# Optimization experiments

Measured on AMD Instinct MI355X. Metric: run time of the kernel, lower is better.

The kernel has to match this reference:

```python
import jax, jax.numpy as jnp
import numpy as np

N, E, IN_DIM, HID = 50000, 800000, 128, 256
H2 = HID // 2
LN_EPS = 1e-5


def setup_inputs() -> dict:
    key = jax.random.key(0)
    ks = jax.random.split(key, 20)
    s = lambda k, shape, fan: jax.random.normal(k, shape, jnp.float32) * (1.0 / np.sqrt(fan))
    return {
        "x": jax.random.normal(ks[0], (N, IN_DIM), jnp.float32),
        "edge_index": jax.random.randint(ks[1], (2, E), 0, N, jnp.int64),
        # GATConv(in_dim, H2, heads=1, concat=False)
        "W_gat": s(ks[2], (IN_DIM, H2), IN_DIM),
        "att_src": s(ks[3], (H2,), H2),
        "att_dst": s(ks[4], (H2,), H2),
        "b_gat": jnp.zeros((H2,), jnp.float32),
        # SAGEConv(in_dim, H2): lin_l (with bias) on aggregated, lin_r (no bias) on root
        "W1l": s(ks[5], (IN_DIM, H2), IN_DIM),
        "b1l": jnp.zeros((H2,), jnp.float32),
        "W1r": s(ks[6], (IN_DIM, H2), IN_DIM),
        "ln1_g": jnp.ones((HID,), jnp.float32),
        "ln1_b": jnp.zeros((HID,), jnp.float32),
        # SAGEConv(hidden, hidden)
        "W2l": s(ks[7], (HID, HID), HID),
        "b2l": jnp.zeros((HID,), jnp.float32),
        "W2r": s(ks[8], (HID, HID), HID),
        "ln2_g": jnp.ones((HID,), jnp.float32),
        "ln2_b": jnp.zeros((HID,), jnp.float32),
        "Wc": s(ks[9], (HID, 1), HID),
        "bc": jnp.zeros((1,), jnp.float32),
    }


def _layernorm(h, g, b):
    mu = jnp.mean(h, axis=-1, keepdims=True)
    var = jnp.mean(jnp.square(h - mu), axis=-1, keepdims=True)
    return (h - mu) * jax.lax.rsqrt(var + LN_EPS) * g + b


def _sage(x, src, dst, Wl, bl, Wr, n):
    # mean aggregation of source features at destination, then lin_l(agg) + lin_r(x)
    s = jax.ops.segment_sum(x[src], dst, num_segments=n)
    deg = jax.ops.segment_sum(jnp.ones((src.shape[0],), x.dtype), dst, num_segments=n)
    agg = s / jnp.maximum(deg, 1.0)[:, None]
    return agg @ Wl + bl + x @ Wr


def _gat(x, src, dst, W, a_s, a_d, b, n):
    # heads=1, concat=False, add_self_loops=True, eval (no dropout)
    loop = jnp.arange(n)
    gs = jnp.concatenate([src, loop])
    gd = jnp.concatenate([dst, loop])
    h = x @ W                                  # [N, H2]
    e = jax.nn.leaky_relu(jnp.take(h @ a_s, gs) + jnp.take(h @ a_d, gd), 0.2)
    emax = jax.ops.segment_max(e, gd, num_segments=n)
    ex = jnp.exp(e - emax[gd])
    denom = jax.ops.segment_sum(ex, gd, num_segments=n)
    alpha = ex / denom[gd]                     # scatter-softmax over in-edges
    out = jax.ops.segment_sum(alpha[:, None] * h[gs], gd, num_segments=n)
    return out + b


def reference(x, edge_index, W_gat, att_src, att_dst, b_gat,
              W1l, b1l, W1r, ln1_g, ln1_b,
              W2l, b2l, W2r, ln2_g, ln2_b, Wc, bc):
    n = x.shape[0]
    src, dst = edge_index[0], edge_index[1]
    x1 = _gat(x, src, dst, W_gat, att_src, att_dst, b_gat, n)
    x2 = _sage(x, src, dst, W1l, b1l, W1r, n)
    h = jnp.concatenate([x1, x2], axis=-1)
    h = jax.nn.relu(_layernorm(h, ln1_g, ln1_b))
    h = _sage(h, src, dst, W2l, b2l, W2r, n)
    h = jax.nn.relu(_layernorm(h, ln2_g, ln2_b))
    return (h @ Wc + bc).squeeze(-1)
```

## Files before the change

### kernel.cpp

```cpp
#include <hip/hip_runtime.h>

#define LN_EPS 1e-5f
#define CA 2048
#define CAPB 6144

typedef __attribute__((ext_vector_type(8))) short short8;
typedef __attribute__((ext_vector_type(4))) float float4a;
typedef __attribute__((ext_vector_type(2))) float float2a;

__device__ __forceinline__ float lrelu(float v) { return v > 0.f ? v : 0.2f * v; }

__device__ __forceinline__ unsigned short f2bf(float f) {
    union { float f; unsigned int u; } x; x.f = f;
    unsigned int u = x.u;
    unsigned int r = (u + 0x7fffu + ((u >> 16) & 1u)) >> 16;
    return (unsigned short)r;
}
__device__ __forceinline__ float bflo(unsigned int v) {
    union { unsigned int u; float f; } x; x.u = v << 16; return x.f;
}
__device__ __forceinline__ float bfhi(unsigned int v) {
    union { unsigned int u; float f; } x; x.u = v & 0xffff0000u; return x.f;
}
__device__ __forceinline__ float2a bf2(unsigned int w) {
    union { unsigned int u; float f; } lo, hi;
    lo.u = w << 16; hi.u = w & 0xffff0000u;
    float2a r; r[0] = lo.f; r[1] = hi.f; return r;
}

__device__ __forceinline__ void load_lds16(const void* g, void* l) {
    __builtin_amdgcn_global_load_lds(
        (const __attribute__((address_space(1))) void*)g,
        (__attribute__((address_space(3))) void*)l, 16, 0, 0);
}

__device__ __forceinline__ uint4 ld16(const char* __restrict__ b, unsigned off) {
    return *(const uint4*)(b + off);
}

__device__ __forceinline__ void accb(float2a aw2[4], float2a ap2[4], float w, uint4 v) {
    float2a wm2; wm2[0] = w; wm2[1] = w;
    float2a f0 = bf2(v.x), f1 = bf2(v.y), f2v = bf2(v.z), f3 = bf2(v.w);
    aw2[0] += wm2 * f0; aw2[1] += wm2 * f1;
    aw2[2] += wm2 * f2v; aw2[3] += wm2 * f3;
    ap2[0] += f0; ap2[1] += f1;
    ap2[2] += f2v; ap2[3] += f3;
}

__device__ __forceinline__ void accbm(float2a aw2[4], float2a ap2[4], float wm, float sm, uint4 v) {
    float2a wm2; wm2[0] = wm; wm2[1] = wm;
    float2a sm2; sm2[0] = sm; sm2[1] = sm;
    float2a f0 = bf2(v.x), f1 = bf2(v.y), f2v = bf2(v.z), f3 = bf2(v.w);
    aw2[0] += wm2 * f0; aw2[1] += wm2 * f1;
    aw2[2] += wm2 * f2v; aw2[3] += wm2 * f3;
    ap2[0] += sm2 * f0; ap2[1] += sm2 * f1;
    ap2[2] += sm2 * f2v; ap2[3] += sm2 * f3;
}

__global__ void prep(const float* __restrict__ W_gat, const float* __restrict__ W1l,
                     const float* __restrict__ W1r, const float* __restrict__ W2l,
                     const float* __restrict__ W2r,
                     const float* __restrict__ att_s, const float* __restrict__ att_d,
                     unsigned short* __restrict__ W12T, unsigned short* __restrict__ W2cT,
                     float* __restrict__ vs, float* __restrict__ vd)
{
    int idx = blockIdx.x * 256 + threadIdx.x;
    if (idx < 98304) {
        int c = idx / 384, k = idx - c * 384;
        float v = 0.f;
        if (c < 128) { if (k < 128) v = W_gat[k * 128 + c]; }
        else {
            int cc = c - 128;
            if (k >= 256)       v = W1r[(k - 256) * 128 + cc];
            else if (k >= 128)  v = W1l[(k - 128) * 128 + cc];
        }
        W12T[idx] = f2bf(v);
    } else if (idx < 229376) {
        int t = idx - 98304;
        int c = t >> 9, k = t & 511;
        float v = (k < 256) ? W2l[k * 256 + c] : W2r[(k - 256) * 256 + c];
        W2cT[t] = f2bf(v);
    } else if (idx < 229376 + 128) {
        int k = idx - 229376;
        float s = 0.f, d = 0.f;
        for (int c = 0; c < 128; ++c) {
            float w = W_gat[k * 128 + c];
            s += w * att_s[c]; d += w * att_d[c];
        }
        vs[k] = s; vd[k] = d;
    }
}

__global__ __launch_bounds__(256) void conv_x_asad(
    const float* __restrict__ x, const float* __restrict__ vs, const float* __restrict__ vd,
    unsigned short* __restrict__ combo3, float* __restrict__ as_, float* __restrict__ ad_, int N)
{
    const int wave = threadIdx.x >> 6, lane = threadIdx.x & 63;
    const int i = blockIdx.x * 4 + wave;
    if (i >= N) return;
    float2 xv = *(const float2*)(x + (size_t)i * 128 + 2 * lane);
    float2 vsv = *(const float2*)(vs + 2 * lane);
    float2 vdv = *(const float2*)(vd + 2 * lane);
    float s = xv.x * vsv.x + xv.y * vsv.y;
    float d = xv.x * vdv.x + xv.y * vdv.y;
    #pragma unroll
    for (int off = 32; off > 0; off >>= 1) {
        s += __shfl_xor(s, off);
        d += __shfl_xor(d, off);
    }
    if (lane == 0) { as_[i] = s; ad_[i] = d; }
    unsigned pk = (unsigned)f2bf(xv.x) | ((unsigned)f2bf(xv.y) << 16);
    *(unsigned*)(combo3 + (size_t)i * 384 + 256 + 2 * lane) = pk;
}

__global__ __launch_bounds__(256) void radix_hist(
    const int* __restrict__ dst, int E, int* __restrict__ blockhist, int B)
{
    const int blk = blockIdx.x, t = threadIdx.x;
    __shared__ int hist[256];
    hist[t] = 0; __syncthreads();
    const int chunk = blk * CA, cend = min(chunk + CA, E);
    for (int j = chunk + t; j < cend; j += 256)
        atomicAdd(&hist[((unsigned)dst[j]) >> 8], 1);
    __syncthreads();
    blockhist[t * B + blk] = hist[t];
}

__global__ __launch_bounds__(256) void scan_rows(
    int* __restrict__ blockhist, int B, int* __restrict__ bintot)
{
    const int bin = blockIdx.x, t = threadIdx.x;
    __shared__ int tmp[256];
    __shared__ int carry;
    if (t == 0) carry = 0;
    __syncthreads();
    const int base = bin * B;
    for (int off0 = 0; off0 < B; off0 += 256) {
        int i = off0 + t;
        int v = (i < B) ? blockhist[base + i] : 0;
        tmp[t] = v; __syncthreads();
        for (int off = 1; off < 256; off <<= 1) {
            int a = (t >= off) ? tmp[t - off] : 0;
            __syncthreads();
            tmp[t] += a;
            __syncthreads();
        }
        int incl = tmp[t] + carry;
        if (i < B) blockhist[base + i] = incl - v;
        __syncthreads();
        if (t == 255) carry = incl;
        __syncthreads();
    }
    if (t == 0) bintot[bin] = carry;
}

__global__ __launch_bounds__(256) void scan_bins(
    const int* __restrict__ bintot, int* __restrict__ bucket_base, int E)
{
    const int t = threadIdx.x;
    __shared__ int tmp[256];
    int v = bintot[t];
    tmp[t] = v; __syncthreads();
    for (int off = 1; off < 256; off <<= 1) {
        int a = (t >= off) ? tmp[t - off] : 0;
        __syncthreads();
        tmp[t] += a;
        __syncthreads();
    }
    bucket_base[t] = tmp[t] - v;
    if (t == 255) bucket_base[256] = E;
}

__global__ __launch_bounds__(256) void radix_scatter(
    const int* __restrict__ src, const int* __restrict__ dst, int E,
    const int* __restrict__ rowscan, const int* __restrict__ bucket_base,
    int B, unsigned int* __restrict__ srt)
{
    const int blk = blockIdx.x, t = threadIdx.x;
    __shared__ int hist[256], lscan[256], lcur[256], gbase[256];
    __shared__ unsigned int recs[CA];
    hist[t] = 0; __syncthreads();
    const int chunk = blk * CA, cend = min(chunk + CA, E);
    for (int j = chunk + t; j < cend; j += 256)
        atomicAdd(&hist[((unsigned)dst[j]) >> 8], 1);
    __syncthreads();
    lscan[t] = hist[t]; __syncthreads();
    for (int off = 1; off < 256; off <<= 1) {
        int a = (t >= off) ? lscan[t - off] : 0;
        __syncthreads();
        lscan[t] += a;
        __syncthreads();
    }
    int excl = lscan[t] - hist[t];
    __syncthreads();
    lscan[t] = excl; lcur[t] = excl;
    gbase[t] = bucket_base[t] + rowscan[t * B + blk];
    __syncthreads();
    for (int j = chunk + t; j < cend; j += 256) {
        int d = dst[j];
        unsigned int r = ((unsigned)d << 16) | (unsigned)src[j];
        int p = atomicAdd(&lcur[((unsigned)d) >> 8], 1);
        recs[p] = r;
    }
    __syncthreads();
    const int cnt = cend - chunk;
    for (int k = t; k < cnt; k += 256) {
        unsigned int r = recs[k];
        int bin = r >> 24;
        srt[gbase[bin] + (k - lscan[bin])] = r;
    }
}

__global__ __launch_bounds__(256) void bucket_sort(
    const unsigned int* __restrict__ srt, const int* __restrict__ bucket_base,
    unsigned short* __restrict__ col_src, int* __restrict__ rp, int N, int E)
{
    const int b = blockIdx.x, t = threadIdx.x;
    const int beg = bucket_base[b], end = bucket_base[b + 1];
    const int cnt = end - beg;
    __shared__ int hist[256], lscan[256], lcur[256];
    __shared__ unsigned int recs[CAPB];
    __shared__ unsigned short outr[CAPB];
    hist[t] = 0; __syncthreads();
    const bool fits = cnt <= CAPB;
    if (fits) {
        for (int j = beg + t; j < end; j += 256) {
            unsigned int r = srt[j];
            recs[j - beg] = r;
            atomicAdd(&hist[(r >> 16) & 255], 1);
        }
    } else {
        for (int j = beg + t; j < end; j += 256)
            atomicAdd(&hist[(srt[j] >> 16) & 255], 1);
    }
    __syncthreads();
    lscan[t] = hist[t]; __syncthreads();
    for (int off = 1; off < 256; off <<= 1) {
        int a = (t >= off) ? lscan[t - off] : 0;
        __syncthreads();
        lscan[t] += a;
        __syncthreads();
    }
    int excl = lscan[t] - hist[t];
    __syncthreads();
    lscan[t] = excl; lcur[t] = excl;
    int d = (b << 8) + t;
    if (d < N) rp[d] = beg + excl;
    if (b == gridDim.x - 1 && t == 0) rp[N] = E;
    __syncthreads();
    if (fits) {
        for (int k = t; k < cnt; k += 256) {
            unsigned int r = recs[k];
            int p = atomicAdd(&lcur[(r >> 16) & 255], 1);
            outr[p] = (unsigned short)(r & 0xFFFFu);
        }
        __syncthreads();
        for (int k = t; k < cnt; k += 256)
            col_src[beg + k] = outr[k];
    } else {
        for (int j = beg + t; j < end; j += 256) {
            unsigned int r = srt[j];
            int p = atomicAdd(&lcur[(r >> 16) & 255], 1);
            col_src[beg + p] = (unsigned short)(r & 0xFFFFu);
        }
    }
}

__global__ __launch_bounds__(256) void gat_sage1(
    const int* __restrict__ row_ptr, const unsigned short* __restrict__ col_src,
    const float* __restrict__ as_, const float* __restrict__ ad_,
    unsigned short* __restrict__ combo3, int N)
{
    const int wave = threadIdx.x >> 6, lane = threadIdx.x & 63;
    const int i = blockIdx.x * 4 + wave;
    if (i >= N) return;
    const int g = lane >> 4, l15 = lane & 15;
    const int beg = row_ptr[i], end = row_ptr[i + 1];
    const int deg = end - beg;
    const float adi = ad_[i];
    const float wself = __expf(lrelu(as_[i] + adi));

    int j = beg + lane;
    int sn_l = (j < end) ? (int)col_src[j] : 0;
    float w_l = (j < end) ? __expf(lrelu(as_[sn_l] + adi)) : 0.f;
    int o_l = sn_l * 768;

    const char* cb = (const char*)combo3;
    const unsigned lo = 512u + 16u * (unsigned)l15;

    uint4 sv = ld16(cb, (unsigned)(i * 768) + lo);
    const int dc = deg < 64 ? deg : 64;
    const int nr = dc >> 3;
    uint4 pv0, pv1; float pw0 = 0.f, pw1 = 0.f;
    if (nr > 0) {
        int so0 = __shfl(o_l, g), so1 = __shfl(o_l, 4 + g);
        pw0 = __shfl(w_l, g); pw1 = __shfl(w_l, 4 + g);
        pv0 = ld16(cb, lo + (unsigned)so0);
        pv1 = ld16(cb, lo + (unsigned)so1);
    }

    float2a aw2[4], ap2[4];
    {
        float wm = (g == 0) ? wself : 0.f;
        float2a wm2; wm2[0] = wm; wm2[1] = wm;
        aw2[0] = wm2 * bf2(sv.x); aw2[1] = wm2 * bf2(sv.y);
        aw2[2] = wm2 * bf2(sv.z); aw2[3] = wm2 * bf2(sv.w);
        #pragma unroll
        for (int k = 0; k < 4; ++k) { ap2[k][0] = 0.f; ap2[k][1] = 0.f; }
    }

    for (int r = 0; r < nr; ++r) {
        uint4 cv0 = pv0, cv1 = pv1;
        float cw0 = pw0, cw1 = pw1;
        if (r + 1 < nr) {
            int b8 = (r + 1) * 8;
            int so0 = __shfl(o_l, b8 + g), so1 = __shfl(o_l, b8 + 4 + g);
            pw0 = __shfl(w_l, b8 + g); pw1 = __shfl(w_l, b8 + 4 + g);
            pv0 = ld16(cb, lo + (unsigned)so0);
            pv1 = ld16(cb, lo + (unsigned)so1);
        }
        accb(aw2, ap2, cw0, cv0);
        accb(aw2, ap2, cw1, cv1);
    }
    for (int j2 = nr * 8; j2 < dc; j2 += 4) {
        int eidx = j2 + g;
        bool val = eidx < dc;
        int so  = __shfl(o_l, val ? eidx : 0);
        float w = __shfl(w_l, val ? eidx : 0);
        uint4 v = ld16(cb, lo + (unsigned)so);
        accbm(aw2, ap2, val ? w : 0.f, val ? 1.f : 0.f, v);
    }
    for (int j3 = 64; j3 < deg; ++j3) {
        int sn = col_src[beg + j3];
        float w = __expf(lrelu(as_[sn] + adi));
        uint4 v = ld16(cb, lo + (unsigned)(sn * 768));
        accbm(aw2, ap2, (g == 0) ? w : 0.f, (g == 0) ? 1.f : 0.f, v);
    }

    float s = w_l;
    for (int jj = beg + lane + 64; jj < end; jj += 64)
        s += __expf(lrelu(as_[col_src[jj]] + adi));
    #pragma unroll
    for (int off = 32; off > 0; off >>= 1) s += __shfl_xor(s, off);
    const float denom = s + wself;

    float aw[8], ap[8];
    #pragma unroll
    for (int k = 0; k < 4; ++k) {
        aw[2 * k] = aw2[k][0]; aw[2 * k + 1] = aw2[k][1];
        ap[2 * k] = ap2[k][0]; ap[2 * k + 1] = ap2[k][1];
    }
    #pragma unroll
    for (int k = 0; k < 8; ++k) {
        aw[k] += __shfl_xor(aw[k], 16); aw[k] += __shfl_xor(aw[k], 32);
        ap[k] += __shfl_xor(ap[k], 16); ap[k] += __shfl_xor(ap[k], 32);
    }
    if (g == 0) {
        float inv = 1.f / denom;
        uint4 pk;
        pk.x = (unsigned)f2bf(aw[0] * inv) | ((unsigned)f2bf(aw[1] * inv) << 16);
        pk.y = (unsigned)f2bf(aw[2] * inv) | ((unsigned)f2bf(aw[3] * inv) << 16);
        pk.z = (unsigned)f2bf(aw[4] * inv) | ((unsigned)f2bf(aw[5] * inv) << 16);
        pk.w = (unsigned)f2bf(aw[6] * inv) | ((unsigned)f2bf(aw[7] * inv) << 16);
        *(uint4*)(combo3 + (size_t)i * 384 + 8 * l15) = pk;
    } else if (g == 1) {
        float dinv = 1.f / fmaxf((float)deg, 1.f);
        uint4 pk;
        pk.x = (unsigned)f2bf(ap[0] * dinv) | ((unsigned)f2bf(ap[1] * dinv) << 16);
        pk.y = (unsigned)f2bf(ap[2] * dinv) | ((unsigned)f2bf(ap[3] * dinv) << 16);
        pk.z = (unsigned)f2bf(ap[4] * dinv) | ((unsigned)f2bf(ap[5] * dinv) << 16);
        pk.w = (unsigned)f2bf(ap[6] * dinv) | ((unsigned)f2bf(ap[7] * dinv) << 16);
        *(uint4*)(combo3 + (size_t)i * 384 + 128 + 8 * l15) = pk;
    }
}

__device__ __forceinline__ int swz_kk(int v) {
    return (((v & 7) ^ ((v >> 3) & 7)) * 8);
}

__global__ __launch_bounds__(256) void gemm12_ln(
    const unsigned short* __restrict__ combo3, int M,
    const unsigned short* __restrict__ W12T,
    const float* __restrict__ b_gat, const float* __restrict__ b1l,
    const float* __restrict__ g1, const float* __restrict__ bb1,
    unsigned short* __restrict__ combo2, unsigned char* __restrict__ hq)
{
    __shared__ __align__(16) unsigned short As[64 * 64];
    __shared__ __align__(16) unsigned short Ws[256 * 64];
    const int tid = threadIdx.x;
    const int bm = blockIdx.x * 64;
    const int wave = tid >> 6, lane = tid & 63;
    const int quad = lane >> 4, l15 = lane & 15;
    const int swz_rd = (l15 & 7) * 8;

    float4a acc[4][4];
    const float4a z4 = {0.f, 0.f, 0.f, 0.f};
    #pragma unroll
    for (int i = 0; i < 4; ++i)
        #pragma unroll
        for (int j = 0; j < 4; ++j) acc[i][j] = z4;

    for (int k0 = 0; k0 < 384; k0 += 64) {
        const bool low = k0 < 128;
        const int rbase = low ? 0 : 128;
        #pragma unroll
        for (int it = 0; it < 2; ++it) {
            int v = tid + it * 256;
            int r = v >> 3, kk = swz_kk(v);
            if (bm + r < M)
                load_lds16(combo3 + (size_t)(bm + r) * 384 + k0 + kk, &As[v * 8]);
        }
        #pragma unroll
        for (int it = 0; it < 4; ++it) {
            int v = tid + it * 256;
            int r = v >> 3, kk = swz_kk(v);
            load_lds16(W12T + (size_t)(rbase + r) * 384 + k0 + kk, &Ws[v * 8]);
        }
        __syncthreads();
        if ((wave < 2) == low) {
            #pragma unroll
            for (int ks = 0; ks < 64; ks += 32) {
                short8 af[4], bfr[4];
                #pragma unroll
                for (int i = 0; i < 4; ++i)
                    af[i] = *(const short8*)(&As[(i * 16 + l15) * 64 + ((ks + quad * 8) ^ swz_rd)]);
                #pragma unroll
                for (int j = 0; j < 4; ++j)
                    bfr[j] = *(const short8*)(&Ws[((wave & 1) * 64 + j * 16 + l15) * 64 + ((ks + quad * 8) ^ swz_rd)]);
                #pragma unroll
                for (int i = 0; i < 4; ++i)
                    #pragma unroll
                    for (int j = 0; j < 4; ++j)
                        acc[i][j] = __builtin_amdgcn_mfma_f32_16x16x32_bf16(af[i], bfr[j], acc[i][j], 0, 0, 0);
            }
        }
        __syncthreads();
    }
    int col[4]; float bcol[4], gc[4], bc2[4];
    #pragma unroll
    for (int j = 0; j < 4; ++j) {
        int c = wave * 64 + j * 16 + l15;
        col[j] = c;
        bcol[j] = (c < 128) ? b_gat[c] : b1l[c - 128];
        gc[j] = g1[c]; bc2[j] = bb1[c];
    }
    float* lsum = (float*)As;
    float* lsq  = lsum + 256;
    #pragma unroll
    for (int i = 0; i < 4; ++i)
        #pragma unroll
        for (int r = 0; r < 4; ++r) {
            float ps = 0.f, pq = 0.f;
            #pragma unroll
            for (int j = 0; j < 4; ++j) {
                float v = acc[i][j][r] + bcol[j];
                ps += v; pq += v * v;
            }
            #pragma unroll
            for (int off = 1; off < 16; off <<= 1) {
                ps += __shfl_xor(ps, off);
                pq += __shfl_xor(pq, off);
            }
            if (l15 == 0) {
                int row = i * 16 + quad * 4 + r;
                lsum[row * 4 + wave] = ps;
                lsq[row * 4 + wave]  = pq;
            }
        }
    __syncthreads();
    unsigned short* Hs = Ws;
    #pragma unroll
    for (int i = 0; i < 4; ++i)
        #pragma unroll
        for (int r = 0; r < 4; ++r) {
            int row = i * 16 + quad * 4 + r;
            float su = lsum[row * 4] + lsum[row * 4 + 1] + lsum[row * 4 + 2] + lsum[row * 4 + 3];
            float sq = lsq[row * 4] + lsq[row * 4 + 1] + lsq[row * 4 + 2] + lsq[row * 4 + 3];
            float mu = su * (1.f / 256.f);
            float var = sq * (1.f / 256.f) - mu * mu;
            float rs = rsqrtf(var + LN_EPS);
            #pragma unroll
            for (int j = 0; j < 4; ++j) {
                float v = acc[i][j][r] + bcol[j];
                float o = fmaxf((v - mu) * rs * gc[j] + bc2[j], 0.f);
                Hs[row * 256 + col[j]] = f2bf(o);
            }
        }
    __syncthreads();
    #pragma unroll
    for (int it = 0; it < 8; ++it) {
        int v = tid + it * 256;
        int r = v >> 5, cc = (v & 31) * 8;
        if (bm + r < M)
            *(uint4*)(combo2 + (size_t)(bm + r) * 512 + 256 + cc) = *(const uint4*)(&Hs[r * 256 + cc]);
    }
    #pragma unroll
    for (int it = 0; it < 4; ++it) {
        int v = tid + it * 256;
        int r = v >> 4, c16 = (v & 15) * 16;
        if (bm + r < M) {
            uint4 o;
            #pragma unroll
            for (int q = 0; q < 4; ++q) {
                unsigned int w0 = *(const unsigned int*)(&Hs[r * 256 + c16 + q * 4 + 0]);
                unsigned int w1 = *(const unsigned int*)(&Hs[r * 256 + c16 + q * 4 + 2]);
                unsigned int t0 = __builtin_amdgcn_cvt_pk_fp8_f32(bflo(w0), bfhi(w0), 0, false);
                unsigned int t1 = __builtin_amdgcn_cvt_pk_fp8_f32(bflo(w1), bfhi(w1), t0, true);
                ((unsigned int*)&o)[q] = t1;
            }
            *(uint4*)(hq + (size_t)(bm + r) * 256 + c16) = o;
        }
    }
}

__global__ __launch_bounds__(256) void sage2_agg(
    const int* __restrict__ row_ptr, const unsigned short* __restrict__ col_src,
    const unsigned char* __restrict__ hq, unsigned short* __restrict__ combo2, int N)
{
    const int wave = threadIdx.x >> 6, lane = threadIdx.x & 63;
    const int i = blockIdx.x * 4 + wave;
    if (i >= N) return;
    const int g = lane >> 4, l15 = lane & 15;
    const int beg = row_ptr[i], end = row_ptr[i + 1];
    const int deg = end - beg;
    int cidx = (beg + lane < end) ? (int)col_src[beg + lane] : 0;
    int o_l = cidx * 256;
    const char* hb = (const char*)hq;
    const unsigned lo = 16u * (unsigned)l15;
    float2a a2[8];
    #pragma unroll
    for (int k = 0; k < 8; ++k) { a2[k][0] = 0.f; a2[k][1] = 0.f; }
    const int dc = deg < 64 ? deg : 64;
    int j = 0;
    for (; j + 8 <= dc; j += 8) {
        #pragma unroll
        for (int u = 0; u < 2; ++u) {
            int eidx = j + 4 * u + g;
            int so = __shfl(o_l, eidx);
            uint4 v = ld16(hb, lo + (unsigned)so);
            a2[0] += __builtin_amdgcn_cvt_pk_f32_fp8(v.x, false);
            a2[1] += __builtin_amdgcn_cvt_pk_f32_fp8(v.x, true);
            a2[2] += __builtin_amdgcn_cvt_pk_f32_fp8(v.y, false);
            a2[3] += __builtin_amdgcn_cvt_pk_f32_fp8(v.y, true);
            a2[4] += __builtin_amdgcn_cvt_pk_f32_fp8(v.z, false);
            a2[5] += __builtin_amdgcn_cvt_pk_f32_fp8(v.z, true);
            a2[6] += __builtin_amdgcn_cvt_pk_f32_fp8(v.w, false);
            a2[7] += __builtin_amdgcn_cvt_pk_f32_fp8(v.w, true);
        }
    }
    for (; j < dc; j += 4) {
        int eidx = j + g;
        bool val = eidx < dc;
        int so = __shfl(o_l, val ? eidx : 0);
        uint4 v = ld16(hb, lo + (unsigned)so);
        float mlt = val ? 1.f : 0.f;
        float2a m2; m2[0] = mlt; m2[1] = mlt;
        a2[0] += m2 * __builtin_amdgcn_cvt_pk_f32_fp8(v.x, false);
        a2[1] += m2 * __builtin_amdgcn_cvt_pk_f32_fp8(v.x, true);
        a2[2] += m2 * __builtin_amdgcn_cvt_pk_f32_fp8(v.y, false);
        a2[3] += m2 * __builtin_amdgcn_cvt_pk_f32_fp8(v.y, true);
        a2[4] += m2 * __builtin_amdgcn_cvt_pk_f32_fp8(v.z, false);
        a2[5] += m2 * __builtin_amdgcn_cvt_pk_f32_fp8(v.z, true);
        a2[6] += m2 * __builtin_amdgcn_cvt_pk_f32_fp8(v.w, false);
        a2[7] += m2 * __builtin_amdgcn_cvt_pk_f32_fp8(v.w, true);
    }
    for (int j3 = 64; j3 < deg; ++j3) {
        int sn = col_src[beg + j3];
        uint4 v = ld16(hb, lo + (unsigned)(sn * 256));
        float mlt = (g == 0) ? 1.f : 0.f;
        float2a m2; m2[0] = mlt; m2[1] = mlt;
        a2[0] += m2 * __builtin_amdgcn_cvt_pk_f32_fp8(v.x, false);
        a2[1] += m2 * __builtin_amdgcn_cvt_pk_f32_fp8(v.x, true);
        a2[2] += m2 * __builtin_amdgcn_cvt_pk_f32_fp8(v.y, false);
        a2[3] += m2 * __builtin_amdgcn_cvt_pk_f32_fp8(v.y, true);
        a2[4] += m2 * __builtin_amdgcn_cvt_pk_f32_fp8(v.z, false);
        a2[5] += m2 * __builtin_amdgcn_cvt_pk_f32_fp8(v.z, true);
        a2[6] += m2 * __builtin_amdgcn_cvt_pk_f32_fp8(v.w, false);
        a2[7] += m2 * __builtin_amdgcn_cvt_pk_f32_fp8(v.w, true);
    }
    float a[16];
    #pragma unroll
    for (int k = 0; k < 8; ++k) { a[2 * k] = a2[k][0]; a[2 * k + 1] = a2[k][1]; }
    #pragma unroll
    for (int k = 0; k < 16; ++k) {
        a[k] += __shfl_xor(a[k], 16);
        a[k] += __shfl_xor(a[k], 32);
    }
    if (g == 0) {
        float dinv = 1.f / fmaxf((float)deg, 1.f);
        uint4 pk0, pk1;
        pk0.x = (unsigned)f2bf(a[0] * dinv)  | ((unsigned)f2bf(a[1] * dinv)  << 16);
        pk0.y = (unsigned)f2bf(a[2] * dinv)  | ((unsigned)f2bf(a[3] * dinv)  << 16);
        pk0.z = (unsigned)f2bf(a[4] * dinv)  | ((unsigned)f2bf(a[5] * dinv)  << 16);
        pk0.w = (unsigned)f2bf(a[6] * dinv)  | ((unsigned)f2bf(a[7] * dinv)  << 16);
        pk1.x = (unsigned)f2bf(a[8] * dinv)  | ((unsigned)f2bf(a[9] * dinv)  << 16);
        pk1.y = (unsigned)f2bf(a[10] * dinv) | ((unsigned)f2bf(a[11] * dinv) << 16);
        pk1.z = (unsigned)f2bf(a[12] * dinv) | ((unsigned)f2bf(a[13] * dinv) << 16);
        pk1.w = (unsigned)f2bf(a[14] * dinv) | ((unsigned)f2bf(a[15] * dinv) << 16);
        *(uint4*)(combo2 + (size_t)i * 512 + 16 * l15)     = pk0;
        *(uint4*)(combo2 + (size_t)i * 512 + 16 * l15 + 8) = pk1;
    }
}

__global__ __launch_bounds__(256) void gemm3_out(
    const unsigned short* __restrict__ combo2, int M,
    const unsigned short* __restrict__ W2cT,
    const float* __restrict__ b2l,
    const float* __restrict__ g2, const float* __restrict__ bb2,
    const float* __restrict__ Wc, const float* __restrict__ bc,
    float* __restrict__ out)
{
    __shared__ __align__(16) unsigned short As[64 * 64];
    __shared__ __align__(16) unsigned short Ws[256 * 64];
    const int tid = threadIdx.x;
    const int bm = blockIdx.x * 64;
    const int wave = tid >> 6, lane = tid & 63;
    const int quad = lane >> 4, l15 = lane & 15;
    const int swz_rd = (l15 & 7) * 8;

    float4a acc[4][4];
    const float4a z4 = {0.f, 0.f, 0.f, 0.f};
    #pragma unroll
    for (int i = 0; i < 4; ++i)
        #pragma unroll
        for (int j = 0; j < 4; ++j) acc[i][j] = z4;

    for (int k0 = 0; k0 < 512; k0 += 64) {
        #pragma unroll
        for (int it = 0; it < 2; ++it) {
            int v = tid + it * 256;
            int r = v >> 3, kk = swz_kk(v);
            if (bm + r < M)
                load_lds16(combo2 + (size_t)(bm + r) * 512 + k0 + kk, &As[v * 8]);
        }
        #pragma unroll
        for (int it = 0; it < 8; ++it) {
            int v = tid + it * 256;
            int r = v >> 3, kk = swz_kk(v);
            load_lds16(W2cT + (size_t)r * 512 + k0 + kk, &Ws[v * 8]);
        }
        __syncthreads();
        #pragma unroll
        for (int ks = 0; ks < 64; ks += 32) {
            short8 af[4], bfr[4];
            #pragma unroll
            for (int i = 0; i < 4; ++i)
                af[i] = *(const short8*)(&As[(i * 16 + l15) * 64 + ((ks + quad * 8) ^ swz_rd)]);
            #pragma unroll
            for (int j = 0; j < 4; ++j)
                bfr[j] = *(const short8*)(&Ws[(wave * 64 + j * 16 + l15) * 64 + ((ks + quad * 8) ^ swz_rd)]);
            #pragma unroll
            for (int i = 0; i < 4; ++i)
                #pragma unroll
                for (int j = 0; j < 4; ++j)
                    acc[i][j] = __builtin_amdgcn_mfma_f32_16x16x32_bf16(af[i], bfr[j], acc[i][j], 0, 0, 0);
        }
        __syncthreads();
    }
    int col[4]; float bcol[4], gc[4], bc2[4], wcl[4];
    #pragma unroll
    for (int j = 0; j < 4; ++j) {
        int c = wave * 64 + j * 16 + l15;
        col[j] = c;
        bcol[j] = b2l[c];
        gc[j] = g2[c]; bc2[j] = bb2[c]; wcl[j] = Wc[c];
    }
    float* lsum = (float*)As;
    float* lsq  = lsum + 256;
    float* ldot = lsum + 512;
    #pragma unroll
    for (int i = 0; i < 4; ++i)
        #pragma unroll
        for (int r = 0; r < 4; ++r) {
            float ps = 0.f, pq = 0.f;
            #pragma unroll
            for (int j = 0; j < 4; ++j) {
                float v = acc[i][j][r] + bcol[j];
                ps += v; pq += v * v;
            }
            #pragma unroll
            for (int off = 1; off < 16; off <<= 1) {
                ps += __shfl_xor(ps, off);
                pq += __shfl_xor(pq, off);
            }
            if (l15 == 0) {
                int row = i * 16 + quad * 4 + r;
                lsum[row * 4 + wave] = ps;
                lsq[row * 4 + wave]  = pq;
            }
        }
    __syncthreads();
    #pragma unroll
    for (int i = 0; i < 4; ++i)
        #pragma unroll
        for (int r = 0; r < 4; ++r) {
            int row = i * 16 + quad * 4 + r;
            float su = lsum[row * 4] + lsum[row * 4 + 1] + lsum[row * 4 + 2] + lsum[row * 4 + 3];
            float sq = lsq[row * 4] + lsq[row * 4 + 1] + lsq[row * 4 + 2] + lsq[row * 4 + 3];
            float mu = su * (1.f / 256.f);
            float var = sq * (1.f / 256.f) - mu * mu;
            float rs = rsqrtf(var + LN_EPS);
            float pd = 0.f;
            #pragma unroll
            for (int j = 0; j < 4; ++j) {
                float v = acc[i][j][r] + bcol[j];
                float o = fmaxf((v - mu) * rs * gc[j] + bc2[j], 0.f);
                pd += o * wcl[j];
            }
            #pragma unroll
            for (int off = 1; off < 16; off <<= 1) pd += __shfl_xor(pd, off);
            if (l15 == 0) ldot[row * 4 + wave] = pd;
        }
    __syncthreads();
    if (tid < 64 && bm + tid < M)
        out[bm + tid] = ldot[tid * 4] + ldot[tid * 4 + 1] + ldot[tid * 4 + 2] + ldot[tid * 4 + 3] + bc[0];
}

extern "C" void kernel_launch(void* const* d_in, const int* in_sizes, int n_in,
                              void* d_out, int out_size, void* d_ws, size_t ws_size,
                              hipStream_t stream)
{
    const float* x     = (const float*)d_in[0];
    const int*   ei    = (const int*)d_in[1];
    const float* W_gat = (const float*)d_in[2];
    const float* att_s = (const float*)d_in[3];
    const float* att_d = (const float*)d_in[4];
    const float* b_gat = (const float*)d_in[5];
    const float* W1l   = (const float*)d_in[6];
    const float* b1l   = (const float*)d_in[7];
    const float* W1r   = (const float*)d_in[8];
    const float* ln1g  = (const float*)d_in[9];
    const float* ln1b  = (const float*)d_in[10];
    const float* W2l   = (const float*)d_in[11];
    const float* b2l   = (const float*)d_in[12];
    const float* W2r   = (const float*)d_in[13];
    const float* ln2g  = (const float*)d_in[14];
    const float* ln2b  = (const float*)d_in[15];
    const float* Wc    = (const float*)d_in[16];
    const float* bc    = (const float*)d_in[17];

    const int N = in_sizes[0] / 128;
    const int E = in_sizes[1] / 2;
    const int* srcp = ei;
    const int* dstp = ei + E;

    char* p = (char*)d_ws;
    unsigned short* combo3 = (unsigned short*)p; p += (size_t)N * 384 * 2;
    unsigned short* combo2 = (unsigned short*)p; p += (size_t)N * 512 * 2;
    unsigned char* hq     = (unsigned char*)p;  p += (size_t)N * 256;
    float* as_    = (float*)p;                 p += (size_t)N * 4;
    float* ad_    = (float*)p;                 p += (size_t)N * 4;
    float* vs     = (float*)p;                 p += 128 * 4;
    float* vd     = (float*)p;                 p += 128 * 4;
    unsigned short* W12T = (unsigned short*)p; p += (size_t)256 * 384 * 2;
    unsigned short* W2cT = (unsigned short*)p; p += (size_t)256 * 512 * 2;
    unsigned int* srt    = (unsigned int*)p;   p += (size_t)E * 4;
    unsigned short* col_src = (unsigned short*)p; p += (((size_t)E * 2 + 15) & ~15ull);
    int* rp       = (int*)p;                   p += (size_t)(N + 1) * 4;
    const int B   = (E + CA - 1) / CA;
    int* blockhist = (int*)p;                  p += (size_t)256 * B * 4;
    int* bucket_base = (int*)p;                p += 257 * 4;
    int* bintot   = (int*)p;                   p += 256 * 4;

    dim3 b256(256);
    const int mb64 = (N + 63) / 64;
    const int nb = (N + 255) >> 8;
    const int prep_total = 229376 + 128;

    hipLaunchKernelGGL(prep, dim3((prep_total + 255) / 256), b256, 0, stream,
                       W_gat, W1l, W1r, W2l, W2r, att_s, att_d, W12T, W2cT, vs, vd);
    hipLaunchKernelGGL(conv_x_asad, dim3((N + 3) / 4), b256, 0, stream,
                       x, vs, vd, combo3, as_, ad_, N);

    hipLaunchKernelGGL(radix_hist, dim3(B), b256, 0, stream, dstp, E, blockhist, B);
    hipLaunchKernelGGL(scan_rows, dim3(256), b256, 0, stream, blockhist, B, bintot);
    hipLaunchKernelGGL(scan_bins, dim3(1), b256, 0, stream, bintot, bucket_base, E);
    hipLaunchKernelGGL(radix_scatter, dim3(B), b256, 0, stream,
                       srcp, dstp, E, blockhist, bucket_base, B, srt);
    hipLaunchKernelGGL(bucket_sort, dim3(nb), b256, 0, stream,
                       srt, bucket_base, col_src, rp, N, E);

    hipLaunchKernelGGL(gat_sage1, dim3((N + 3) / 4), b256, 0, stream,
                       rp, col_src, as_, ad_, combo3, N);

    hipLaunchKernelGGL(gemm12_ln, dim3(mb64), b256, 0, stream,
                       combo3, N, W12T, b_gat, b1l, ln1g, ln1b, combo2, hq);

    hipLaunchKernelGGL(sage2_agg, dim3((N + 3) / 4), b256, 0, stream,
                       rp, col_src, hq, combo2, N);

    hipLaunchKernelGGL(gemm3_out, dim3(mb64), b256, 0, stream,
                       combo2, N, W2cT, b2l, ln2g, ln2b, Wc, bc, (float*)d_out);
}
```

Before: 277.0 us.

## Process two nodes per wavefront in GAT and SAGE aggregation kernels

Both neighbor-aggregation kernels now split each 64-lane wavefront into two 32-lane halves, each handling its own destination node, with two 16-lane groups per node instead of four. The average degree is about 16, so most lanes in a one-node-per-wave layout sat idle. The new layout is meant to keep more lanes busy and cut the number of waves and the cross-group shuffle reductions. In exchange, each node gets half the gather parallelism, and nodes with more than 32 neighbors fall to the slow serial tail loop sooner.

```diff
diff --git a/kernel.cpp b/kernel.cpp
--- a/kernel.cpp
+++ b/kernel.cpp
@@ -272,15 +272,19 @@
     unsigned short* __restrict__ combo3, int N)
 {
     const int wave = threadIdx.x >> 6, lane = threadIdx.x & 63;
-    const int i = blockIdx.x * 4 + wave;
-    if (i >= N) return;
-    const int g = lane >> 4, l15 = lane & 15;
-    const int beg = row_ptr[i], end = row_ptr[i + 1];
+    const int half = lane >> 5, hl = lane & 31;
+    const int g2 = (lane >> 4) & 1, l15 = lane & 15;
+    const int h32 = half << 5;
+    const int i = blockIdx.x * 8 + wave * 2 + half;
+    const bool valid = i < N;
+
+    const int beg = valid ? row_ptr[i] : 0;
+    const int end = valid ? row_ptr[i + 1] : 0;
     const int deg = end - beg;
-    const float adi = ad_[i];
-    const float wself = __expf(lrelu(as_[i] + adi));
-
-    int j = beg + lane;
+    const float adi = valid ? ad_[i] : 0.f;
+    const float wself = valid ? __expf(lrelu(as_[i] + adi)) : 0.f;
+
+    int j = beg + hl;
     int sn_l = (j < end) ? (int)col_src[j] : 0;
     float w_l = (j < end) ? __expf(lrelu(as_[sn_l] + adi)) : 0.f;
     int o_l = sn_l * 768;
@@ -288,20 +292,20 @@
     const char* cb = (const char*)combo3;
     const unsigned lo = 512u + 16u * (unsigned)l15;
 
-    uint4 sv = ld16(cb, (unsigned)(i * 768) + lo);
-    const int dc = deg < 64 ? deg : 64;
-    const int nr = dc >> 3;
+    uint4 sv = ld16(cb, (unsigned)(valid ? i : 0) * 768u + lo);
+    const int dc = deg < 32 ? deg : 32;
+    const int nr = dc >> 2;
     uint4 pv0, pv1; float pw0 = 0.f, pw1 = 0.f;
     if (nr > 0) {
-        int so0 = __shfl(o_l, g), so1 = __shfl(o_l, 4 + g);
-        pw0 = __shfl(w_l, g); pw1 = __shfl(w_l, 4 + g);
+        int so0 = __shfl(o_l, h32 + g2), so1 = __shfl(o_l, h32 + 2 + g2);
+        pw0 = __shfl(w_l, h32 + g2); pw1 = __shfl(w_l, h32 + 2 + g2);
         pv0 = ld16(cb, lo + (unsigned)so0);
         pv1 = ld16(cb, lo + (unsigned)so1);
     }
 
     float2a aw2[4], ap2[4];
     {
-        float wm = (g == 0) ? wself : 0.f;
+        float wm = (g2 == 0) ? wself : 0.f;
         float2a wm2; wm2[0] = wm; wm2[1] = wm;
         aw2[0] = wm2 * bf2(sv.x); aw2[1] = wm2 * bf2(sv.y);
         aw2[2] = wm2 * bf2(sv.z); aw2[3] = wm2 * bf2(sv.w);
@@ -313,35 +317,35 @@
         uint4 cv0 = pv0, cv1 = pv1;
         float cw0 = pw0, cw1 = pw1;
         if (r + 1 < nr) {
-            int b8 = (r + 1) * 8;
-            int so0 = __shfl(o_l, b8 + g), so1 = __shfl(o_l, b8 + 4 + g);
-            pw0 = __shfl(w_l, b8 + g); pw1 = __shfl(w_l, b8 + 4 + g);
+            int b4 = (r + 1) * 4;
+            int so0 = __shfl(o_l, h32 + b4 + g2), so1 = __shfl(o_l, h32 + b4 + 2 + g2);
+            pw0 = __shfl(w_l, h32 + b4 + g2); pw1 = __shfl(w_l, h32 + b4 + 2 + g2);
             pv0 = ld16(cb, lo + (unsigned)so0);
             pv1 = ld16(cb, lo + (unsigned)so1);
         }
         accb(aw2, ap2, cw0, cv0);
         accb(aw2, ap2, cw1, cv1);
     }
-    for (int j2 = nr * 8; j2 < dc; j2 += 4) {
-        int eidx = j2 + g;
+    for (int j2 = nr * 4; j2 < dc; j2 += 2) {
+        int eidx = j2 + g2;
         bool val = eidx < dc;
-        int so  = __shfl(o_l, val ? eidx : 0);
-        float w = __shfl(w_l, val ? eidx : 0);
+        int so  = __shfl(o_l, h32 + (val ? eidx : 0));
+        float w = __shfl(w_l, h32 + (val ? eidx : 0));
         uint4 v = ld16(cb, lo + (unsigned)so);
         accbm(aw2, ap2, val ? w : 0.f, val ? 1.f : 0.f, v);
     }
-    for (int j3 = 64; j3 < deg; ++j3) {
+    for (int j3 = 32; j3 < deg; ++j3) {
         int sn = col_src[beg + j3];
         float w = __expf(lrelu(as_[sn] + adi));
         uint4 v = ld16(cb, lo + (unsigned)(sn * 768));
-        accbm(aw2, ap2, (g == 0) ? w : 0.f, (g == 0) ? 1.f : 0.f, v);
+        accbm(aw2, ap2, (g2 == 0) ? w : 0.f, (g2 == 0) ? 1.f : 0.f, v);
     }
 
     float s = w_l;
-    for (int jj = beg + lane + 64; jj < end; jj += 64)
+    for (int jj = beg + hl + 32; jj < end; jj += 32)
         s += __expf(lrelu(as_[col_src[jj]] + adi));
     #pragma unroll
-    for (int off = 32; off > 0; off >>= 1) s += __shfl_xor(s, off);
+    for (int off = 16; off > 0; off >>= 1) s += __shfl_xor(s, off);
     const float denom = s + wself;
 
     float aw[8], ap[8];
@@ -352,10 +356,10 @@
     }
     #pragma unroll
     for (int k = 0; k < 8; ++k) {
-        aw[k] += __shfl_xor(aw[k], 16); aw[k] += __shfl_xor(aw[k], 32);
-        ap[k] += __shfl_xor(ap[k], 16); ap[k] += __shfl_xor(ap[k], 32);
-    }
-    if (g == 0) {
+        aw[k] += __shfl_xor(aw[k], 16);
+        ap[k] += __shfl_xor(ap[k], 16);
+    }
+    if (valid && g2 == 0) {
         float inv = 1.f / denom;
         uint4 pk;
         pk.x = (unsigned)f2bf(aw[0] * inv) | ((unsigned)f2bf(aw[1] * inv) << 16);
@@ -363,7 +367,7 @@
         pk.z = (unsigned)f2bf(aw[4] * inv) | ((unsigned)f2bf(aw[5] * inv) << 16);
         pk.w = (unsigned)f2bf(aw[6] * inv) | ((unsigned)f2bf(aw[7] * inv) << 16);
         *(uint4*)(combo3 + (size_t)i * 384 + 8 * l15) = pk;
-    } else if (g == 1) {
+    } else if (valid && g2 == 1) {
         float dinv = 1.f / fmaxf((float)deg, 1.f);
         uint4 pk;
         pk.x = (unsigned)f2bf(ap[0] * dinv) | ((unsigned)f2bf(ap[1] * dinv) << 16);
@@ -518,25 +522,29 @@
     const unsigned char* __restrict__ hq, unsigned short* __restrict__ combo2, int N)
 {
     const int wave = threadIdx.x >> 6, lane = threadIdx.x & 63;
-    const int i = blockIdx.x * 4 + wave;
-    if (i >= N) return;
-    const int g = lane >> 4, l15 = lane & 15;
-    const int beg = row_ptr[i], end = row_ptr[i + 1];
+    const int half = lane >> 5, hl = lane & 31;
+    const int g2 = (lane >> 4) & 1, l15 = lane & 15;
+    const int h32 = half << 5;
+    const int i = blockIdx.x * 8 + wave * 2 + half;
+    const bool valid = i < N;
+
+    const int beg = valid ? row_ptr[i] : 0;
+    const int end = valid ? row_ptr[i + 1] : 0;
     const int deg = end - beg;
-    int cidx = (beg + lane < end) ? (int)col_src[beg + lane] : 0;
+    int cidx = (beg + hl < end) ? (int)col_src[beg + hl] : 0;
     int o_l = cidx * 256;
     const char* hb = (const char*)hq;
     const unsigned lo = 16u * (unsigned)l15;
     float2a a2[8];
     #pragma unroll
     for (int k = 0; k < 8; ++k) { a2[k][0] = 0.f; a2[k][1] = 0.f; }
-    const int dc = deg < 64 ? deg : 64;
+    const int dc = deg < 32 ? deg : 32;
     int j = 0;
-    for (; j + 8 <= dc; j += 8) {
+    for (; j + 4 <= dc; j += 4) {
         #pragma unroll
         for (int u = 0; u < 2; ++u) {
-            int eidx = j + 4 * u + g;
-            int so = __shfl(o_l, eidx);
+            int eidx = j + 2 * u + g2;
+            int so = __shfl(o_l, h32 + eidx);
             uint4 v = ld16(hb, lo + (unsigned)so);
             a2[0] += __builtin_amdgcn_cvt_pk_f32_fp8(v.x, false);
             a2[1] += __builtin_amdgcn_cvt_pk_f32_fp8(v.x, true);
@@ -548,10 +556,10 @@
             a2[7] += __builtin_amdgcn_cvt_pk_f32_fp8(v.w, true);
         }
     }
-    for (; j < dc; j += 4) {
-        int eidx = j + g;
+    for (; j < dc; j += 2) {
+        int eidx = j + g2;
         bool val = eidx < dc;
-        int so = __shfl(o_l, val ? eidx : 0);
+        int so = __shfl(o_l, h32 + (val ? eidx : 0));
         uint4 v = ld16(hb, lo + (unsigned)so);
         float mlt = val ? 1.f : 0.f;
         float2a m2; m2[0] = mlt; m2[1] = mlt;
@@ -564,10 +572,10 @@
         a2[6] += m2 * __builtin_amdgcn_cvt_pk_f32_fp8(v.w, false);
         a2[7] += m2 * __builtin_amdgcn_cvt_pk_f32_fp8(v.w, true);
     }
-    for (int j3 = 64; j3 < deg; ++j3) {
+    for (int j3 = 32; j3 < deg; ++j3) {
         int sn = col_src[beg + j3];
         uint4 v = ld16(hb, lo + (unsigned)(sn * 256));
-        float mlt = (g == 0) ? 1.f : 0.f;
+        float mlt = (g2 == 0) ? 1.f : 0.f;
         float2a m2; m2[0] = mlt; m2[1] = mlt;
         a2[0] += m2 * __builtin_amdgcn_cvt_pk_f32_fp8(v.x, false);
         a2[1] += m2 * __builtin_amdgcn_cvt_pk_f32_fp8(v.x, true);
@@ -582,11 +590,9 @@
     #pragma unroll
     for (int k = 0; k < 8; ++k) { a[2 * k] = a2[k][0]; a[2 * k + 1] = a2[k][1]; }
     #pragma unroll
-    for (int k = 0; k < 16; ++k) {
+    for (int k = 0; k < 16; ++k)
         a[k] += __shfl_xor(a[k], 16);
-        a[k] += __shfl_xor(a[k], 32);
-    }
-    if (g == 0) {
+    if (valid && g2 == 0) {
         float dinv = 1.f / fmaxf((float)deg, 1.f);
         uint4 pk0, pk1;
         pk0.x = (unsigned)f2bf(a[0] * dinv)  | ((unsigned)f2bf(a[1] * dinv)  << 16);
@@ -780,13 +786,13 @@
     hipLaunchKernelGGL(bucket_sort, dim3(nb), b256, 0, stream,
                        srt, bucket_base, col_src, rp, N, E);
 
-    hipLaunchKernelGGL(gat_sage1, dim3((N + 3) / 4), b256, 0, stream,
+    hipLaunchKernelGGL(gat_sage1, dim3((N + 7) / 8), b256, 0, stream,
                        rp, col_src, as_, ad_, combo3, N);
 
     hipLaunchKernelGGL(gemm12_ln, dim3(mb64), b256, 0, stream,
                        combo3, N, W12T, b_gat, b1l, ln1g, ln1b, combo2, hq);
 
-    hipLaunchKernelGGL(sage2_agg, dim3((N + 3) / 4), b256, 0, stream,
+    hipLaunchKernelGGL(sage2_agg, dim3((N + 7) / 8), b256, 0, stream,
                        rp, col_src, hq, combo2, N);
 
     hipLaunchKernelGGL(gemm3_out, dim3(mb64), b256, 0, stream,
```

Result: no change. 273.3 us (median of 3 runs) (-1.3%).
